# Kernel optimization log

Measured on AMD Instinct MI355X. Metric: run time of the kernel, lower is better.

The kernel has to match this reference:

```python
import jax, jax.numpy as jnp
import numpy as np

N_NODES = 50000
NEG_SLOPE = 0.2


def gat_layer(x, src, dst, edge_attr, W, a_src, a_dst, We, a_edge, b, n):
    """PyG GATConv (heads=1, concat=True, add_self_loops=True, fill_value='mean')."""
    h = x @ W                                   # [N, C] shared lin for src/dst
    alpha_s = h @ a_src                          # [N]
    alpha_d = h @ a_dst                          # [N]
    # self loops; self-loop edge_attr = mean of incoming edge_attr per node
    deg = jax.ops.segment_sum(jnp.ones_like(dst, dtype=edge_attr.dtype), dst, num_segments=n)
    ea_mean = jax.ops.segment_sum(edge_attr, dst, num_segments=n) / jnp.maximum(deg, 1.0)[:, None]
    loop = jnp.arange(n, dtype=src.dtype)
    s = jnp.concatenate([src, loop])             # [E+N]
    d = jnp.concatenate([dst, loop])
    ea = jnp.concatenate([edge_attr, ea_mean], axis=0)
    alpha_e = (ea @ We) @ a_edge                 # [E+N]
    alpha = jax.nn.leaky_relu(alpha_s[s] + alpha_d[d] + alpha_e, NEG_SLOPE)
    # segment softmax over destination neighborhoods (self-loops guarantee non-empty)
    amax = jax.ops.segment_max(alpha, d, num_segments=n)
    ealpha = jnp.exp(alpha - amax[d])
    denom = jax.ops.segment_sum(ealpha, d, num_segments=n)
    coef = ealpha / denom[d]                     # [E+N]
    out = jax.ops.segment_sum(h[s] * coef[:, None], d, num_segments=n)
    return out + b


def setup_inputs() -> dict:
    key = jax.random.key(0)
    ks = jax.random.split(key, 16)
    N, E, F_in, H, C, ED = N_NODES, 800000, 256, 128, 128, 60
    inp = {
        "x": jax.random.normal(ks[0], (N, F_in), jnp.float32),
        "edge_index": jax.random.randint(ks[1], (2, E), 0, N, jnp.int32),
        "edge_features": jax.random.normal(ks[2], (E, ED), jnp.float32),
        "batch_size": 16,
    }
    def glorot(k, shape):
        fan = shape[0] + (shape[1] if len(shape) > 1 else 1)
        return jax.random.normal(k, shape, jnp.float32) * np.sqrt(2.0 / fan)
    # layer 1
    inp["W1"] = glorot(ks[3], (F_in, H))
    inp["a_src1"] = glorot(ks[4], (H,))
    inp["a_dst1"] = glorot(ks[5], (H,))
    inp["We1"] = glorot(ks[6], (ED, H))
    inp["a_edge1"] = glorot(ks[7], (H,))
    inp["b1"] = jnp.zeros((H,), jnp.float32)
    # layer 2
    inp["W2"] = glorot(ks[8], (H, C))
    inp["a_src2"] = glorot(ks[9], (C,))
    inp["a_dst2"] = glorot(ks[10], (C,))
    inp["We2"] = glorot(ks[11], (ED, C))
    inp["a_edge2"] = glorot(ks[12], (C,))
    inp["b2"] = jnp.zeros((C,), jnp.float32)
    return inp


def reference(x, edge_index, edge_features, batch_size,
              W1, a_src1, a_dst1, We1, a_edge1, b1,
              W2, a_src2, a_dst2, We2, a_edge2, b2):
    n = x.shape[0]
    src, dst = edge_index[0], edge_index[1]
    h = gat_layer(x, src, dst, edge_features, W1, a_src1, a_dst1, We1, a_edge1, b1, n)
    h = jax.nn.relu(h)
    z = gat_layer(h, src, dst, edge_features, W2, a_src2, a_dst2, We2, a_edge2, b2, n)
    # decode: gather-dot over labeled edge pairs
    res = jnp.sum(z[src] * z[dst], axis=-1)      # [E]
    half = res.shape[0] // 2
    res_half = res[:half] + res[half:]
    return res_half.reshape((batch_size, -1))
```

## Files before the change

kernel.cpp:

```cpp
#include <hip/hip_runtime.h>
#include <hip/hip_bf16.h>

typedef __attribute__((ext_vector_type(8))) short short8;
typedef __attribute__((ext_vector_type(4))) float floatx4;

__device__ __forceinline__ float wsum(float v){
  #pragma unroll
  for (int m = 32; m >= 1; m >>= 1) v += __shfl_xor(v, m);
  return v;
}
__device__ __forceinline__ float lrelu(float a){ return a > 0.f ? a : 0.2f * a; }
__device__ __forceinline__ float bflo(unsigned u){ return __uint_as_float(u << 16); }
__device__ __forceinline__ float bfhi(unsigned u){ return __uint_as_float(u & 0xffff0000u); }
__device__ __forceinline__ unsigned short f2bf(float f){
  __hip_bfloat16 h = __float2bfloat16(f);
  return *reinterpret_cast<unsigned short*>(&h);
}

__global__ __launch_bounds__(256) void k_prep(const float* __restrict__ We1, const float* __restrict__ ae1,
                       const float* __restrict__ We2, const float* __restrict__ ae2,
                       float* __restrict__ we1, float* __restrict__ we2,
                       const float* __restrict__ W1, unsigned short* __restrict__ W1t,
                       const float* __restrict__ W2, unsigned short* __restrict__ W2t) {
  int b = blockIdx.x, t = threadIdx.x;
  if (b == 0) {
    if (t >= 64) return;
    float s1 = 0.f, s2 = 0.f;
    if (t < 60) {
      const float4* r1 = reinterpret_cast<const float4*>(We1 + t * 128);
      const float4* r2 = reinterpret_cast<const float4*>(We2 + t * 128);
      const float4* a1 = reinterpret_cast<const float4*>(ae1);
      const float4* a2 = reinterpret_cast<const float4*>(ae2);
      for (int i = 0; i < 32; ++i) {
        float4 x1 = r1[i], y1 = a1[i];
        float4 x2 = r2[i], y2 = a2[i];
        s1 += x1.x*y1.x + x1.y*y1.y + x1.z*y1.z + x1.w*y1.w;
        s2 += x2.x*y2.x + x2.y*y2.y + x2.z*y2.z + x2.w*y2.w;
      }
    }
    we1[t] = s1; we2[t] = s2;
  } else if (b <= 128) {
    int idx = (b - 1) * 256 + t;
    int k = idx >> 7, n = idx & 127;
    W1t[(size_t)n * 256 + k] = f2bf(W1[idx]);
  } else {
    int idx = (b - 129) * 256 + t;
    int k = idx >> 7, n = idx & 127;
    W2t[(size_t)n * 128 + k] = f2bf(W2[idx]);
  }
}

__global__ void k_count(const int* __restrict__ dst, int* __restrict__ degi,
                        int* __restrict__ eslot, int E) {
  int e = blockIdx.x * blockDim.x + threadIdx.x;
  if (e < E) eslot[e] = atomicAdd(degi + dst[e], 1);
}

__global__ __launch_bounds__(1024) void k_scan(const int* __restrict__ degi, int* __restrict__ rowptr,
                                               int N, int E) {
  __shared__ int part[1024];
  int t = threadIdx.x;
  const int CH = 52;
  int lo = t * CH;
  int v[52];
  int s = 0;
  #pragma unroll
  for (int i = 0; i < 13; ++i) {
    int base_i = lo + 4 * i;
    if (base_i + 4 <= N) {
      int4 q = *reinterpret_cast<const int4*>(degi + base_i);
      v[4*i+0] = q.x; v[4*i+1] = q.y; v[4*i+2] = q.z; v[4*i+3] = q.w;
      s += q.x + q.y + q.z + q.w;
    } else {
      #pragma unroll
      for (int j = 0; j < 4; ++j) {
        int idx = base_i + j;
        int x = (idx < N) ? degi[idx] : 0;
        v[4*i+j] = x; s += x;
      }
    }
  }
  part[t] = s;
  __syncthreads();
  for (int off = 1; off < 1024; off <<= 1) {
    int u = (t >= off) ? part[t - off] : 0;
    __syncthreads();
    part[t] += u;
    __syncthreads();
  }
  int base = (t == 0) ? 0 : part[t - 1];
  #pragma unroll
  for (int i = 0; i < 13; ++i) {
    int base_i = lo + 4 * i;
    if (base_i + 4 <= N) {
      int4 o;
      o.x = base; base += v[4*i+0];
      o.y = base; base += v[4*i+1];
      o.z = base; base += v[4*i+2];
      o.w = base; base += v[4*i+3];
      *reinterpret_cast<int4*>(rowptr + base_i) = o;
    } else {
      #pragma unroll
      for (int j = 0; j < 4; ++j) {
        int idx = base_i + j;
        if (idx < N) { rowptr[idx] = base; base += v[4*i+j]; }
      }
    }
  }
  if (t == 0) rowptr[N] = E;
}

__global__ __launch_bounds__(256) void k_fill(const int* __restrict__ src, const int* __restrict__ dst,
                       const float* __restrict__ ef,
                       const float* __restrict__ we1, const float* __restrict__ we2,
                       const int* __restrict__ rowptr, const int* __restrict__ eslot,
                       float4* __restrict__ csr, int E) {
  __shared__ float w1[64], w2[64];
  int t = threadIdx.x;
  if (t < 64) { w1[t] = we1[t]; w2[t] = we2[t]; }
  __syncthreads();
  int gid = blockIdx.x * 256 + t;
  int e = gid >> 2;
  int sub = gid & 3;
  if (e >= E) return;
  const float4* row = reinterpret_cast<const float4*>(ef + (size_t)e * 60);
  float d1 = 0.f, d2 = 0.f;
  #pragma unroll
  for (int i = sub; i < 15; i += 4) {
    float4 f = row[i];
    d1 += f.x*w1[4*i] + f.y*w1[4*i+1] + f.z*w1[4*i+2] + f.w*w1[4*i+3];
    d2 += f.x*w2[4*i] + f.y*w2[4*i+1] + f.z*w2[4*i+2] + f.w*w2[4*i+3];
  }
  d1 += __shfl_xor(d1, 1); d1 += __shfl_xor(d1, 2);
  d2 += __shfl_xor(d2, 1); d2 += __shfl_xor(d2, 2);
  if (sub == 0) {
    int d = dst[e];
    int slot = rowptr[d] + eslot[e];
    float4 v;
    v.x = __int_as_float(src[e]); v.y = d1; v.z = d2; v.w = 0.f;
    csr[slot] = v;
  }
}

template <int K, bool AFP32>
__global__ __launch_bounds__(256) void k_gemm(const void* __restrict__ Av, const unsigned short* __restrict__ Bt,
                                              unsigned short* __restrict__ C,
                                              const float* __restrict__ a_src, const float* __restrict__ a_dst,
                                              float* __restrict__ alps, float* __restrict__ alpd, int M) {
  int wid = (blockIdx.x * 256 + threadIdx.x) >> 6;
  int lane = threadIdx.x & 63;
  int mt = wid >> 1, hf = wid & 1;
  if (mt * 16 >= M) return;
  int r = lane & 15, quad = lane >> 4;
  int m = mt * 16 + r;
  floatx4 acc[4] = {};
  for (int k0 = 0; k0 < K; k0 += 32) {
    int kk = k0 + quad * 8;
    short8 a;
    if (AFP32) {
      const float4* ap = reinterpret_cast<const float4*>((const float*)Av + (size_t)m * K + kk);
      float4 lo = ap[0], hi = ap[1];
      union { short8 v; unsigned short u[8]; } pa;
      pa.u[0]=f2bf(lo.x); pa.u[1]=f2bf(lo.y); pa.u[2]=f2bf(lo.z); pa.u[3]=f2bf(lo.w);
      pa.u[4]=f2bf(hi.x); pa.u[5]=f2bf(hi.y); pa.u[6]=f2bf(hi.z); pa.u[7]=f2bf(hi.w);
      a = pa.v;
    } else {
      a = *reinterpret_cast<const short8*>((const unsigned short*)Av + (size_t)m * K + kk);
    }
    #pragma unroll
    for (int t = 0; t < 4; ++t) {
      short8 b = *reinterpret_cast<const short8*>(Bt + (size_t)(hf*64 + t*16 + r) * K + kk);
      acc[t] = __builtin_amdgcn_mfma_f32_16x16x32_bf16(a, b, acc[t], 0, 0, 0);
    }
  }
  float asv[4], adv[4];
  #pragma unroll
  for (int t = 0; t < 4; ++t) {
    int col = hf * 64 + t * 16 + r;
    asv[t] = a_src[col]; adv[t] = a_dst[col];
  }
  #pragma unroll
  for (int rr = 0; rr < 4; ++rr) {
    float ps = 0.f, pd = 0.f;
    #pragma unroll
    for (int t = 0; t < 4; ++t) { ps += acc[t][rr] * asv[t]; pd += acc[t][rr] * adv[t]; }
    #pragma unroll
    for (int mo = 1; mo <= 8; mo <<= 1) { ps += __shfl_xor(ps, mo); pd += __shfl_xor(pd, mo); }
    if (r == 0) {
      int row = mt * 16 + quad * 4 + rr;
      atomicAdd(alps + row, ps);
      atomicAdd(alpd + row, pd);
    }
  }
  #pragma unroll
  for (int t = 0; t < 4; ++t) {
    int col = hf * 64 + t * 16 + r;
    #pragma unroll
    for (int rr = 0; rr < 4; ++rr) {
      int row = mt * 16 + quad * 4 + rr;
      C[(size_t)row * 128 + col] = f2bf(acc[t][rr]);
    }
  }
}

__global__ __launch_bounds__(256) void k_agg(const int* __restrict__ rowptr, const float4* __restrict__ csr,
                      const float* __restrict__ as_, const float* __restrict__ ad_,
                      const unsigned short* __restrict__ h, const float* __restrict__ bias,
                      unsigned short* __restrict__ out, int N, int use2, int do_relu) {
  int i = (blockIdx.x * blockDim.x + threadIdx.x) >> 6;
  int lane = threadIdx.x & 63;
  if (i >= N) return;
  int st = lane >> 4;
  int q  = lane & 15;
  int start = rowptr[i], end = rowptr[i + 1];
  int cnt = end - start;
  float adi = ad_[i], asi = as_[i];
  float m = -3.0e38f, s = 0.f, esum = 0.f;
  float acc[8] = {};
  int idx = start + st;
  float4 cur, nx;
  float as_c = 0.f; uint4 hv_c;
  if (idx < end) {
    cur = csr[idx];
    int sv = __float_as_int(cur.x);
    as_c = as_[sv];
    hv_c = *reinterpret_cast<const uint4*>(h + (size_t)sv * 128 + q * 8);
  }
  if (idx + 4 < end) nx = csr[idx + 4];
  for (; idx < end; idx += 4) {
    float4 n2;
    if (idx + 8 < end) n2 = csr[idx + 8];
    float as_n = 0.f; uint4 hv_n;
    if (idx + 4 < end) {
      int svn = __float_as_int(nx.x);
      as_n = as_[svn];
      hv_n = *reinterpret_cast<const uint4*>(h + (size_t)svn * 128 + q * 8);
    }
    float e = use2 ? cur.z : cur.y;
    float a = lrelu(as_c + adi + e);
    esum += e;
    if (a > m + 8.f) {
      float rr = __expf(m - a);
      s *= rr;
      #pragma unroll
      for (int j = 0; j < 8; ++j) acc[j] *= rr;
      m = a;
    }
    float w = __expf(a - m);
    s += w;
    acc[0] += w * bflo(hv_c.x); acc[1] += w * bfhi(hv_c.x);
    acc[2] += w * bflo(hv_c.y); acc[3] += w * bfhi(hv_c.y);
    acc[4] += w * bflo(hv_c.z); acc[5] += w * bfhi(hv_c.z);
    acc[6] += w * bflo(hv_c.w); acc[7] += w * bfhi(hv_c.w);
    cur = nx; nx = n2; as_c = as_n; hv_c = hv_n;
  }
  #pragma unroll
  for (int off = 16; off <= 32; off <<= 1) {
    float m_o = __shfl_xor(m, off);
    float s_o = __shfl_xor(s, off);
    float e_o = __shfl_xor(esum, off);
    float ao[8];
    #pragma unroll
    for (int j = 0; j < 8; ++j) ao[j] = __shfl_xor(acc[j], off);
    float Mn = fmaxf(m, m_o);
    float f  = __expf(m - Mn), fo = __expf(m_o - Mn);
    s = s * f + s_o * fo;
    #pragma unroll
    for (int j = 0; j < 8; ++j) acc[j] = acc[j] * f + ao[j] * fo;
    esum += e_o;
    m = Mn;
  }
  float a_self = lrelu(asi + adi + esum / fmaxf((float)cnt, 1.f));
  float M2 = fmaxf(m, a_self);
  float g = __expf(m - M2);
  float w_self = __expf(a_self - M2);
  s = s * g + w_self;
  uint4 hs = *reinterpret_cast<const uint4*>(h + (size_t)i * 128 + q * 8);
  float hsf[8] = { bflo(hs.x), bfhi(hs.x), bflo(hs.y), bfhi(hs.y),
                   bflo(hs.z), bfhi(hs.z), bflo(hs.w), bfhi(hs.w) };
  #pragma unroll
  for (int j = 0; j < 8; ++j) acc[j] = acc[j] * g + w_self * hsf[j];
  float inv = 1.0f / s;
  float4 bv0 = *reinterpret_cast<const float4*>(bias + q * 8);
  float4 bv1 = *reinterpret_cast<const float4*>(bias + q * 8 + 4);
  float o[8];
  o[0] = acc[0]*inv + bv0.x; o[1] = acc[1]*inv + bv0.y;
  o[2] = acc[2]*inv + bv0.z; o[3] = acc[3]*inv + bv0.w;
  o[4] = acc[4]*inv + bv1.x; o[5] = acc[5]*inv + bv1.y;
  o[6] = acc[6]*inv + bv1.z; o[7] = acc[7]*inv + bv1.w;
  if (do_relu) {
    #pragma unroll
    for (int j = 0; j < 8; ++j) o[j] = fmaxf(o[j], 0.f);
  }
  if (st == 0) {
    uint4 ov;
    ov.x = (unsigned)f2bf(o[0]) | ((unsigned)f2bf(o[1]) << 16);
    ov.y = (unsigned)f2bf(o[2]) | ((unsigned)f2bf(o[3]) << 16);
    ov.z = (unsigned)f2bf(o[4]) | ((unsigned)f2bf(o[5]) << 16);
    ov.w = (unsigned)f2bf(o[6]) | ((unsigned)f2bf(o[7]) << 16);
    *reinterpret_cast<uint4*>(out + (size_t)i * 128 + q * 8) = ov;
  }
}

__global__ void k_decode(const int* __restrict__ src, const int* __restrict__ dst,
                         const unsigned short* __restrict__ z, float* __restrict__ out, int halfE) {
  int w = (blockIdx.x * blockDim.x + threadIdx.x) >> 6;
  int lane = threadIdx.x & 63;
  int k0 = w * 2;
  if (k0 >= halfE) return;
  int sel = lane >> 4;
  int q = lane & 15;
  int k = k0 + (sel >> 1), hh = sel & 1;
  float p = 0.f;
  if (k < halfE) {
    int e = k + hh * halfE;
    int sv = src[e], dv = dst[e];
    uint4 a = *reinterpret_cast<const uint4*>(z + (size_t)sv * 128 + q * 8);
    uint4 b = *reinterpret_cast<const uint4*>(z + (size_t)dv * 128 + q * 8);
    p = bflo(a.x)*bflo(b.x) + bfhi(a.x)*bfhi(b.x)
      + bflo(a.y)*bflo(b.y) + bfhi(a.y)*bfhi(b.y)
      + bflo(a.z)*bflo(b.z) + bfhi(a.z)*bfhi(b.z)
      + bflo(a.w)*bflo(b.w) + bfhi(a.w)*bfhi(b.w);
  }
  #pragma unroll
  for (int mo = 1; mo <= 16; mo <<= 1) p += __shfl_xor(p, mo);
  float p1 = __shfl(p, 32);
  if (lane == 0) {
    if (k0 + 2 <= halfE) {
      *reinterpret_cast<float2*>(out + k0) = make_float2(p, p1);
    } else {
      out[k0] = p;
    }
  }
}

extern "C" void kernel_launch(void* const* d_in, const int* in_sizes, int n_in,
                              void* d_out, int out_size, void* d_ws, size_t ws_size,
                              hipStream_t stream) {
  const int H = 128;
  const int N = in_sizes[0] / 256;
  const int E = in_sizes[1] / 2;
  const int half = E / 2;

  const float* x   = (const float*)d_in[0];
  const int* eidx  = (const int*)d_in[1];
  const float* ef  = (const float*)d_in[2];
  const float* W1  = (const float*)d_in[4];
  const float* as1 = (const float*)d_in[5];
  const float* ad1 = (const float*)d_in[6];
  const float* We1 = (const float*)d_in[7];
  const float* ae1 = (const float*)d_in[8];
  const float* b1  = (const float*)d_in[9];
  const float* W2  = (const float*)d_in[10];
  const float* as2 = (const float*)d_in[11];
  const float* ad2 = (const float*)d_in[12];
  const float* We2 = (const float*)d_in[13];
  const float* ae2 = (const float*)d_in[14];
  const float* b2  = (const float*)d_in[15];

  const int* src = eidx;
  const int* dst = eidx + E;

  size_t off = 0;
  auto alloc = [&](size_t bytes) -> void* {
    void* p = (char*)d_ws + off;
    off += (bytes + 255) & ~(size_t)255;
    return p;
  };
  float*  we1    = (float*)alloc(64 * 4);
  float*  we2    = (float*)alloc(64 * 4);
  int*    zeroblk= (int*)alloc((size_t)N * 4 * 5);
  int*    degi   = zeroblk;
  float*  alps1  = (float*)(zeroblk + (size_t)N);
  float*  alpd1  = (float*)(zeroblk + (size_t)2 * N);
  float*  alps2  = (float*)(zeroblk + (size_t)3 * N);
  float*  alpd2  = (float*)(zeroblk + (size_t)4 * N);
  int*    eslot  = (int*)alloc((size_t)E * 4);
  int*    rowptr = (int*)alloc((size_t)(N + 1) * 4);
  float4* csr    = (float4*)alloc((size_t)E * 16);
  unsigned short* W1t = (unsigned short*)alloc((size_t)128 * 256 * 2);
  unsigned short* W2t = (unsigned short*)alloc((size_t)128 * 128 * 2);
  unsigned short* hA  = (unsigned short*)alloc((size_t)N * H * 2);
  unsigned short* hB  = (unsigned short*)alloc((size_t)N * H * 2);

  hipMemsetAsync(zeroblk, 0, (size_t)N * 4 * 5, stream);

  k_prep<<<193, 256, 0, stream>>>(We1, ae1, We2, ae2, we1, we2, W1, W1t, W2, W2t);
  k_count<<<(E + 255) / 256, 256, 0, stream>>>(dst, degi, eslot, E);
  k_scan<<<1, 1024, 0, stream>>>(degi, rowptr, N, E);
  k_fill<<<(E * 4 + 255) / 256, 256, 0, stream>>>(src, dst, ef, we1, we2, rowptr, eslot, csr, E);

  int gwaves = ((N + 15) / 16) * 2;
  int gblocks = (gwaves + 3) / 4;
  k_gemm<256, true><<<gblocks, 256, 0, stream>>>(x, W1t, hA, as1, ad1, alps1, alpd1, N);
  k_agg<<<(N + 3) / 4, 256, 0, stream>>>(rowptr, csr, alps1, alpd1, hA, b1, hB, N, 0, 1);
  k_gemm<128, false><<<gblocks, 256, 0, stream>>>(hB, W2t, hA, as2, ad2, alps2, alpd2, N);
  k_agg<<<(N + 3) / 4, 256, 0, stream>>>(rowptr, csr, alps2, alpd2, hA, b2, hB, N, 1, 0);
  int dwaves = (half + 1) / 2;
  k_decode<<<(dwaves + 3) / 4, 256, 0, stream>>>(src, dst, hB, (float*)d_out, half);
}
```

Before: 591.4 us.

## Merge prep/count and fill/gemm launches, wave-shuffle scan, full-width GEMM waves

Folds the edge-count atomics into the prep kernel and the CSR fill into the first GEMM launch as separate block ranges, cutting kernel launches. The single-block scan now uses wave shuffles instead of a 1024-step shared-memory loop with many barriers. Each GEMM wave now computes all 128 columns, so attention logits are stored directly instead of atomically added. This shrinks the memset and reuses one alps/alpd buffer for both layers. In exchange it doubles accumulator registers per wave and halves the number of GEMM waves.

After: 556.6 us. -5.9%, faster.

```diff
diff --git a/kernel.cpp b/kernel.cpp
--- a/kernel.cpp
+++ b/kernel.cpp
@@ -17,12 +17,20 @@
   return *reinterpret_cast<unsigned short*>(&h);
 }
 
-__global__ __launch_bounds__(256) void k_prep(const float* __restrict__ We1, const float* __restrict__ ae1,
+__global__ __launch_bounds__(256) void k_prep(const int* __restrict__ dst, int* __restrict__ degi,
+                       int* __restrict__ eslot, int E, int CB,
+                       const float* __restrict__ We1, const float* __restrict__ ae1,
                        const float* __restrict__ We2, const float* __restrict__ ae2,
                        float* __restrict__ we1, float* __restrict__ we2,
                        const float* __restrict__ W1, unsigned short* __restrict__ W1t,
                        const float* __restrict__ W2, unsigned short* __restrict__ W2t) {
-  int b = blockIdx.x, t = threadIdx.x;
+  int t = threadIdx.x;
+  if (blockIdx.x < (unsigned)CB) {
+    int e = blockIdx.x * 256 + t;
+    if (e < E) eslot[e] = atomicAdd(degi + dst[e], 1);
+    return;
+  }
+  int b = blockIdx.x - CB;
   if (b == 0) {
     if (t >= 64) return;
     float s1 = 0.f, s2 = 0.f;
@@ -50,16 +58,11 @@
   }
 }
 
-__global__ void k_count(const int* __restrict__ dst, int* __restrict__ degi,
-                        int* __restrict__ eslot, int E) {
-  int e = blockIdx.x * blockDim.x + threadIdx.x;
-  if (e < E) eslot[e] = atomicAdd(degi + dst[e], 1);
-}
-
 __global__ __launch_bounds__(1024) void k_scan(const int* __restrict__ degi, int* __restrict__ rowptr,
                                                int N, int E) {
-  __shared__ int part[1024];
+  __shared__ int wsums[16];
   int t = threadIdx.x;
+  int wave = t >> 6, lane = t & 63;
   const int CH = 52;
   int lo = t * CH;
   int v[52];
@@ -80,15 +83,25 @@
       }
     }
   }
-  part[t] = s;
+  int inc = s;
+  #pragma unroll
+  for (int off = 1; off < 64; off <<= 1) {
+    int u = __shfl_up(inc, off);
+    if (lane >= off) inc += u;
+  }
+  if (lane == 63) wsums[wave] = inc;
   __syncthreads();
-  for (int off = 1; off < 1024; off <<= 1) {
-    int u = (t >= off) ? part[t - off] : 0;
-    __syncthreads();
-    part[t] += u;
-    __syncthreads();
-  }
-  int base = (t == 0) ? 0 : part[t - 1];
+  if (wave == 0) {
+    int ws = (lane < 16) ? wsums[lane] : 0;
+    #pragma unroll
+    for (int off = 1; off < 16; off <<= 1) {
+      int u = __shfl_up(ws, off);
+      if (lane >= off) ws += u;
+    }
+    if (lane < 16) wsums[lane] = ws;
+  }
+  __syncthreads();
+  int base = inc - s + (wave ? wsums[wave - 1] : 0);
   #pragma unroll
   for (int i = 0; i < 13; ++i) {
     int base_i = lo + 4 * i;
@@ -110,50 +123,17 @@
   if (t == 0) rowptr[N] = E;
 }
 
-__global__ __launch_bounds__(256) void k_fill(const int* __restrict__ src, const int* __restrict__ dst,
-                       const float* __restrict__ ef,
-                       const float* __restrict__ we1, const float* __restrict__ we2,
-                       const int* __restrict__ rowptr, const int* __restrict__ eslot,
-                       float4* __restrict__ csr, int E) {
-  __shared__ float w1[64], w2[64];
-  int t = threadIdx.x;
-  if (t < 64) { w1[t] = we1[t]; w2[t] = we2[t]; }
-  __syncthreads();
-  int gid = blockIdx.x * 256 + t;
-  int e = gid >> 2;
-  int sub = gid & 3;
-  if (e >= E) return;
-  const float4* row = reinterpret_cast<const float4*>(ef + (size_t)e * 60);
-  float d1 = 0.f, d2 = 0.f;
-  #pragma unroll
-  for (int i = sub; i < 15; i += 4) {
-    float4 f = row[i];
-    d1 += f.x*w1[4*i] + f.y*w1[4*i+1] + f.z*w1[4*i+2] + f.w*w1[4*i+3];
-    d2 += f.x*w2[4*i] + f.y*w2[4*i+1] + f.z*w2[4*i+2] + f.w*w2[4*i+3];
-  }
-  d1 += __shfl_xor(d1, 1); d1 += __shfl_xor(d1, 2);
-  d2 += __shfl_xor(d2, 1); d2 += __shfl_xor(d2, 2);
-  if (sub == 0) {
-    int d = dst[e];
-    int slot = rowptr[d] + eslot[e];
-    float4 v;
-    v.x = __int_as_float(src[e]); v.y = d1; v.z = d2; v.w = 0.f;
-    csr[slot] = v;
-  }
-}
-
 template <int K, bool AFP32>
-__global__ __launch_bounds__(256) void k_gemm(const void* __restrict__ Av, const unsigned short* __restrict__ Bt,
-                                              unsigned short* __restrict__ C,
-                                              const float* __restrict__ a_src, const float* __restrict__ a_dst,
-                                              float* __restrict__ alps, float* __restrict__ alpd, int M) {
-  int wid = (blockIdx.x * 256 + threadIdx.x) >> 6;
-  int lane = threadIdx.x & 63;
-  int mt = wid >> 1, hf = wid & 1;
+__device__ __forceinline__ void gemm_body(int wid, int lane,
+    const void* __restrict__ Av, const unsigned short* __restrict__ Bt,
+    unsigned short* __restrict__ C,
+    const float* __restrict__ a_src, const float* __restrict__ a_dst,
+    float* __restrict__ alps, float* __restrict__ alpd, int M) {
+  int mt = wid;
   if (mt * 16 >= M) return;
   int r = lane & 15, quad = lane >> 4;
   int m = mt * 16 + r;
-  floatx4 acc[4] = {};
+  floatx4 acc[8] = {};
   for (int k0 = 0; k0 < K; k0 += 32) {
     int kk = k0 + quad * 8;
     short8 a;
@@ -168,38 +148,91 @@
       a = *reinterpret_cast<const short8*>((const unsigned short*)Av + (size_t)m * K + kk);
     }
     #pragma unroll
-    for (int t = 0; t < 4; ++t) {
-      short8 b = *reinterpret_cast<const short8*>(Bt + (size_t)(hf*64 + t*16 + r) * K + kk);
+    for (int t = 0; t < 8; ++t) {
+      short8 b = *reinterpret_cast<const short8*>(Bt + (size_t)(t*16 + r) * K + kk);
       acc[t] = __builtin_amdgcn_mfma_f32_16x16x32_bf16(a, b, acc[t], 0, 0, 0);
     }
   }
-  float asv[4], adv[4];
-  #pragma unroll
-  for (int t = 0; t < 4; ++t) {
-    int col = hf * 64 + t * 16 + r;
+  float asv[8], adv[8];
+  #pragma unroll
+  for (int t = 0; t < 8; ++t) {
+    int col = t * 16 + r;
     asv[t] = a_src[col]; adv[t] = a_dst[col];
   }
   #pragma unroll
   for (int rr = 0; rr < 4; ++rr) {
     float ps = 0.f, pd = 0.f;
     #pragma unroll
-    for (int t = 0; t < 4; ++t) { ps += acc[t][rr] * asv[t]; pd += acc[t][rr] * adv[t]; }
+    for (int t = 0; t < 8; ++t) { ps += acc[t][rr] * asv[t]; pd += acc[t][rr] * adv[t]; }
     #pragma unroll
     for (int mo = 1; mo <= 8; mo <<= 1) { ps += __shfl_xor(ps, mo); pd += __shfl_xor(pd, mo); }
     if (r == 0) {
       int row = mt * 16 + quad * 4 + rr;
-      atomicAdd(alps + row, ps);
-      atomicAdd(alpd + row, pd);
-    }
-  }
-  #pragma unroll
-  for (int t = 0; t < 4; ++t) {
-    int col = hf * 64 + t * 16 + r;
+      alps[row] = ps;
+      alpd[row] = pd;
+    }
+  }
+  #pragma unroll
+  for (int t = 0; t < 8; ++t) {
+    int col = t * 16 + r;
     #pragma unroll
     for (int rr = 0; rr < 4; ++rr) {
       int row = mt * 16 + quad * 4 + rr;
       C[(size_t)row * 128 + col] = f2bf(acc[t][rr]);
     }
+  }
+}
+
+template <int K, bool AFP32>
+__global__ __launch_bounds__(256) void k_gemm(const void* __restrict__ Av, const unsigned short* __restrict__ Bt,
+                                              unsigned short* __restrict__ C,
+                                              const float* __restrict__ a_src, const float* __restrict__ a_dst,
+                                              float* __restrict__ alps, float* __restrict__ alpd, int M) {
+  int wid = (blockIdx.x * 256 + threadIdx.x) >> 6;
+  int lane = threadIdx.x & 63;
+  gemm_body<K, AFP32>(wid, lane, Av, Bt, C, a_src, a_dst, alps, alpd, M);
+}
+
+__global__ __launch_bounds__(256) void k_fillgemm(
+                       const int* __restrict__ src, const int* __restrict__ dst,
+                       const float* __restrict__ ef,
+                       const float* __restrict__ we1, const float* __restrict__ we2,
+                       const int* __restrict__ rowptr, const int* __restrict__ eslot,
+                       float4* __restrict__ csr, int E, int GB,
+                       const float* __restrict__ x, const unsigned short* __restrict__ W1t,
+                       unsigned short* __restrict__ hA,
+                       const float* __restrict__ a_src, const float* __restrict__ a_dst,
+                       float* __restrict__ alps, float* __restrict__ alpd, int N) {
+  __shared__ float w1[64], w2[64];
+  int t = threadIdx.x;
+  if (blockIdx.x < (unsigned)GB) {
+    int wid = (blockIdx.x * 256 + t) >> 6;
+    int lane = t & 63;
+    gemm_body<256, true>(wid, lane, x, W1t, hA, a_src, a_dst, alps, alpd, N);
+    return;
+  }
+  if (t < 64) { w1[t] = we1[t]; w2[t] = we2[t]; }
+  __syncthreads();
+  int gid = (blockIdx.x - GB) * 256 + t;
+  int e = gid >> 2;
+  int sub = gid & 3;
+  if (e >= E) return;
+  const float4* row = reinterpret_cast<const float4*>(ef + (size_t)e * 60);
+  float d1 = 0.f, d2 = 0.f;
+  #pragma unroll
+  for (int i = sub; i < 15; i += 4) {
+    float4 f = row[i];
+    d1 += f.x*w1[4*i] + f.y*w1[4*i+1] + f.z*w1[4*i+2] + f.w*w1[4*i+3];
+    d2 += f.x*w2[4*i] + f.y*w2[4*i+1] + f.z*w2[4*i+2] + f.w*w2[4*i+3];
+  }
+  d1 += __shfl_xor(d1, 1); d1 += __shfl_xor(d1, 2);
+  d2 += __shfl_xor(d2, 1); d2 += __shfl_xor(d2, 2);
+  if (sub == 0) {
+    int d = dst[e];
+    int slot = rowptr[d] + eslot[e];
+    float4 v;
+    v.x = __int_as_float(src[e]); v.y = d1; v.z = d2; v.w = 0.f;
+    csr[slot] = v;
   }
 }
 
@@ -369,12 +402,9 @@
   };
   float*  we1    = (float*)alloc(64 * 4);
   float*  we2    = (float*)alloc(64 * 4);
-  int*    zeroblk= (int*)alloc((size_t)N * 4 * 5);
-  int*    degi   = zeroblk;
-  float*  alps1  = (float*)(zeroblk + (size_t)N);
-  float*  alpd1  = (float*)(zeroblk + (size_t)2 * N);
-  float*  alps2  = (float*)(zeroblk + (size_t)3 * N);
-  float*  alpd2  = (float*)(zeroblk + (size_t)4 * N);
+  int*    degi   = (int*)alloc((size_t)N * 4);
+  float*  alps   = (float*)alloc((size_t)N * 4);
+  float*  alpd   = (float*)alloc((size_t)N * 4);
   int*    eslot  = (int*)alloc((size_t)E * 4);
   int*    rowptr = (int*)alloc((size_t)(N + 1) * 4);
   float4* csr    = (float4*)alloc((size_t)E * 16);
@@ -383,19 +413,21 @@
   unsigned short* hA  = (unsigned short*)alloc((size_t)N * H * 2);
   unsigned short* hB  = (unsigned short*)alloc((size_t)N * H * 2);
 
-  hipMemsetAsync(zeroblk, 0, (size_t)N * 4 * 5, stream);
-
-  k_prep<<<193, 256, 0, stream>>>(We1, ae1, We2, ae2, we1, we2, W1, W1t, W2, W2t);
-  k_count<<<(E + 255) / 256, 256, 0, stream>>>(dst, degi, eslot, E);
+  hipMemsetAsync(degi, 0, (size_t)N * 4, stream);
+
+  int CB = (E + 255) / 256;
+  k_prep<<<CB + 193, 256, 0, stream>>>(dst, degi, eslot, E, CB,
+                                       We1, ae1, We2, ae2, we1, we2, W1, W1t, W2, W2t);
   k_scan<<<1, 1024, 0, stream>>>(degi, rowptr, N, E);
-  k_fill<<<(E * 4 + 255) / 256, 256, 0, stream>>>(src, dst, ef, we1, we2, rowptr, eslot, csr, E);
-
-  int gwaves = ((N + 15) / 16) * 2;
-  int gblocks = (gwaves + 3) / 4;
-  k_gemm<256, true><<<gblocks, 256, 0, stream>>>(x, W1t, hA, as1, ad1, alps1, alpd1, N);
-  k_agg<<<(N + 3) / 4, 256, 0, stream>>>(rowptr, csr, alps1, alpd1, hA, b1, hB, N, 0, 1);
-  k_gemm<128, false><<<gblocks, 256, 0, stream>>>(hB, W2t, hA, as2, ad2, alps2, alpd2, N);
-  k_agg<<<(N + 3) / 4, 256, 0, stream>>>(rowptr, csr, alps2, alpd2, hA, b2, hB, N, 1, 0);
+
+  int gwaves = (N + 15) / 16;
+  int GB = (gwaves + 3) / 4;
+  int FB = (E * 4 + 255) / 256;
+  k_fillgemm<<<GB + FB, 256, 0, stream>>>(src, dst, ef, we1, we2, rowptr, eslot, csr, E, GB,
+                                          x, W1t, hA, as1, ad1, alps, alpd, N);
+  k_agg<<<(N + 3) / 4, 256, 0, stream>>>(rowptr, csr, alps, alpd, hA, b1, hB, N, 0, 1);
+  k_gemm<128, false><<<GB, 256, 0, stream>>>(hB, W2t, hA, as2, ad2, alps, alpd, N);
+  k_agg<<<(N + 3) / 4, 256, 0, stream>>>(rowptr, csr, alps, alpd, hA, b2, hB, N, 1, 0);
   int dwaves = (half + 1) / 2;
   k_decode<<<(dwaves + 3) / 4, 256, 0, stream>>>(src, dst, hB, (float*)d_out, half);
 }
```
